# Performance work log

Measured on AMD Instinct MI355X. Metric: run time of the kernel, lower is better.

Reference implementation:

```python
import jax, jax.numpy as jnp
import numpy as np

N = 50000      # nodes
E = 500000     # edges (before self-loops)
D = 384        # in_channels == hidden3*6 (residual constraint)
H1, C1 = 4, 96   # conv1: heads, out_channels  -> 384
H2, C2 = 4, 96   # conv2 -> 384
H3, C3 = 6, 64   # conv3 -> 384
B = 64           # graphs in batch
SLOPE = 0.2      # GATConv leaky_relu negative_slope (PyG default)
LN_EPS = 1e-5


def _gat_params(key, fin, heads, c, scale=0.05):
    k1, k2, k3 = jax.random.split(key, 3)
    return dict(
        W=jax.random.normal(k1, (fin, heads * c), jnp.float32) * scale,
        a_src=jax.random.normal(k2, (heads, c), jnp.float32) * scale,
        a_dst=jax.random.normal(k3, (heads, c), jnp.float32) * scale,
        b=jnp.zeros((heads * c,), jnp.float32),
    )


def setup_inputs() -> dict:
    key = jax.random.key(0)
    ks = jax.random.split(key, 8)
    x = jax.random.normal(ks[0], (N, D), jnp.float32)
    edge_index = jax.random.randint(ks[1], (2, E), 0, N).astype(jnp.int64)
    batch = jnp.sort(jax.random.randint(ks[2], (N,), 0, B)).astype(jnp.int64)
    p1 = _gat_params(ks[3], D, H1, C1)
    p2 = _gat_params(ks[4], H1 * C1, H2, C2)
    p3 = _gat_params(ks[5], H2 * C2, H3, C3)
    return {
        'x': x, 'edge_index': edge_index, 'batch': batch,
        'W1': p1['W'], 'a1_src': p1['a_src'], 'a1_dst': p1['a_dst'], 'b1': p1['b'],
        'g1': jnp.ones((H1 * C1,), jnp.float32), 'be1': jnp.zeros((H1 * C1,), jnp.float32),
        'W2': p2['W'], 'a2_src': p2['a_src'], 'a2_dst': p2['a_dst'], 'b2': p2['b'],
        'g2': jnp.ones((H2 * C2,), jnp.float32), 'be2': jnp.zeros((H2 * C2,), jnp.float32),
        'W3': p3['W'], 'a3_src': p3['a_src'], 'a3_dst': p3['a_dst'], 'b3': p3['b'],
    }


def _layer_norm(x, g, b):
    mu = jnp.mean(x, axis=-1, keepdims=True)
    var = jnp.mean(jnp.square(x - mu), axis=-1, keepdims=True)
    return (x - mu) * jax.lax.rsqrt(var + LN_EPS) * g + b


def _gat_conv(x, src, dst, W, a_src, a_dst, b, heads, c):
    # h: [N, H, C] projected features (shared W across heads, PyG-style)
    h = (x @ W).reshape(N, heads, c)
    s_src = jnp.einsum('nhc,hc->nh', h, a_src)   # [N, H]
    s_dst = jnp.einsum('nhc,hc->nh', h, a_dst)
    e = jax.nn.leaky_relu(s_src[src] + s_dst[dst], SLOPE)  # [E', H]
    # segment softmax over incoming edges of each dst (self-loops guarantee coverage)
    e_max = jax.ops.segment_max(e, dst, num_segments=N)
    e = jnp.exp(e - e_max[dst])
    denom = jax.ops.segment_sum(e, dst, num_segments=N)
    alpha = e / (denom[dst] + 1e-16)                        # [E', H]
    out = jax.ops.segment_sum(h[src] * alpha[:, :, None], dst, num_segments=N)
    return out.reshape(N, heads * c) + b


def reference(x, edge_index, batch,
              W1, a1_src, a1_dst, b1, g1, be1,
              W2, a2_src, a2_dst, b2, g2, be2,
              W3, a3_src, a3_dst, b3):
    # PyG GATConv adds self-loops by default
    ar = jnp.arange(N, dtype=edge_index.dtype)
    ei = jnp.concatenate([edge_index, jnp.stack([ar, ar])], axis=1)
    src, dst = ei[0], ei[1]

    x1 = _gat_conv(x, src, dst, W1, a1_src, a1_dst, b1, H1, C1)
    x1 = jax.nn.relu(_layer_norm(x1, g1, be1))
    x2 = _gat_conv(x1, src, dst, W2, a2_src, a2_dst, b2, H2, C2)
    x2 = jax.nn.relu(_layer_norm(x2, g2, be2))
    x3 = _gat_conv(x2, src, dst, W3, a3_src, a3_dst, b3, H3, C3)
    x3 = jax.nn.relu(x3)

    x_res = x + x3
    # global_mean_pool over batch assignment (dropout is identity at eval)
    sums = jax.ops.segment_sum(x_res, batch, num_segments=B)
    counts = jax.ops.segment_sum(jnp.ones((N,), x.dtype), batch, num_segments=B)
    return sums / jnp.maximum(counts, 1.0)[:, None]
```

## Files before the change

### kernel.cpp

```cpp
#include <hip/hip_runtime.h>

#define NNODES 50000
#define NEDGES 500000
#define DIM    384
#define NB     64
#define SLOPE  0.2f
#define LN_EPS 1e-5f
#define EPRIME (NEDGES + NNODES)
#define POOLS  16
#define SCANB  256
#define NSCB   ((NNODES + SCANB - 1) / SCANB)

typedef __attribute__((ext_vector_type(8))) short short8;
typedef __attribute__((ext_vector_type(4))) float floatx4;
typedef __attribute__((ext_vector_type(2))) float floatx2;

__device__ __forceinline__ int load_i(const void* p, long long i, int is64) {
  return is64 ? (int)((const long long*)p)[i] : ((const int*)p)[i];
}
__device__ __forceinline__ unsigned short f2bf(float f) {
  unsigned u = __float_as_uint(f);
  u += 0x7fffu + ((u >> 16) & 1u);
  return (unsigned short)(u >> 16);
}
__device__ __forceinline__ float bf2f(unsigned short u) {
  return __uint_as_float(((unsigned)u) << 16);
}

__global__ void detect_kernel(const int* __restrict__ ei32, int* __restrict__ flag) {
  __shared__ int nz;
  if (threadIdx.x == 0) nz = 0;
  __syncthreads();
  if (ei32[2 * threadIdx.x + 1] != 0) atomicAdd(&nz, 1);
  __syncthreads();
  if (threadIdx.x == 0) *flag = (nz == 0) ? 1 : 0;
}

__global__ void count_kernel(const void* __restrict__ ei, const int* __restrict__ flag,
                             int* __restrict__ deg) {
  int is64 = *flag;
  for (int i = blockIdx.x * blockDim.x + threadIdx.x; i < EPRIME; i += gridDim.x * blockDim.x) {
    int d = (i < NEDGES) ? load_i(ei, (long long)NEDGES + i, is64) : (i - NEDGES);
    atomicAdd(&deg[d], 1);
  }
}

__global__ void scan1_kernel(const int* __restrict__ deg, int* __restrict__ row_ptr,
                             int* __restrict__ btot) {
  __shared__ int buf[SCANB];
  int t = threadIdx.x, idx = blockIdx.x * SCANB + t;
  int v = (idx < NNODES) ? deg[idx] : 0;
  buf[t] = v;
  __syncthreads();
  for (int off = 1; off < SCANB; off <<= 1) {
    int x = (t >= off) ? buf[t - off] : 0;
    __syncthreads();
    buf[t] += x;
    __syncthreads();
  }
  if (idx < NNODES) row_ptr[idx] = buf[t] - v;
  if (t == SCANB - 1) btot[blockIdx.x] = buf[t];
}
__global__ void scan2_kernel(int* __restrict__ btot) {
  __shared__ int buf[256];
  int t = threadIdx.x;
  int v = (t < NSCB) ? btot[t] : 0;
  buf[t] = v;
  __syncthreads();
  for (int off = 1; off < 256; off <<= 1) {
    int x = (t >= off) ? buf[t - off] : 0;
    __syncthreads();
    buf[t] += x;
    __syncthreads();
  }
  if (t < NSCB) btot[t] = buf[t] - v;
}
__global__ void scan3_kernel(int* __restrict__ row_ptr, int* __restrict__ cursor,
                             const int* __restrict__ btot) {
  int idx = blockIdx.x * SCANB + threadIdx.x;
  if (idx < NNODES) {
    int v = row_ptr[idx] + btot[blockIdx.x];
    row_ptr[idx] = v;
    cursor[idx] = v;
  }
  if (idx == 0) row_ptr[NNODES] = EPRIME;
}

__global__ void scatter_kernel(const void* __restrict__ ei, const int* __restrict__ flag,
                               int* __restrict__ cursor, int* __restrict__ srt) {
  int is64 = *flag;
  for (int i = blockIdx.x * blockDim.x + threadIdx.x; i < EPRIME; i += gridDim.x * blockDim.x) {
    int s, d;
    if (i < NEDGES) { s = load_i(ei, i, is64); d = load_i(ei, (long long)NEDGES + i, is64); }
    else            { s = d = i - NEDGES; }
    int pos = atomicAdd(&cursor[d], 1);
    srt[pos] = s;
  }
}

__global__ void convert_x_kernel(const float* __restrict__ x, unsigned short* __restrict__ xb) {
  int i = blockIdx.x * blockDim.x + threadIdx.x;
  float4 v = ((const float4*)x)[i];
  ushort4 o;
  o.x = f2bf(v.x); o.y = f2bf(v.y); o.z = f2bf(v.z); o.w = f2bf(v.w);
  ((ushort4*)xb)[i] = o;
}

__global__ void convert_w_kernel(const float* __restrict__ W1, const float* __restrict__ W2,
                                 const float* __restrict__ W3, unsigned short* __restrict__ Wt) {
  const float* W = (blockIdx.y == 0) ? W1 : (blockIdx.y == 1) ? W2 : W3;
  unsigned short* o = Wt + (size_t)blockIdx.y * DIM * DIM;
  int n = blockIdx.x;
  int k = threadIdx.x;
  o[n * DIM + k] = f2bf(W[k * DIM + n]);
}

__global__ __launch_bounds__(256)
void gemm_bf16_kernel(const unsigned short* __restrict__ A,
                      const unsigned short* __restrict__ Bt,
                      unsigned short* __restrict__ Cb, int M) {
  __shared__ unsigned short As[128 * 32];
  __shared__ unsigned short Bs[128 * 32];
  int tid = threadIdx.x;
  int lane = tid & 63;
  int wave = tid >> 6;
  int bm = blockIdx.x * 128;
  int bn = blockIdx.y * 128;
  int wm = (wave & 1) * 64;
  int wn = (wave >> 1) * 64;
  int l16 = lane & 15;
  int lq  = lane >> 4;

  floatx4 acc[4][4];
#pragma unroll
  for (int mi = 0; mi < 4; ++mi)
#pragma unroll
    for (int ni = 0; ni < 4; ++ni)
      acc[mi][ni] = (floatx4){0.f, 0.f, 0.f, 0.f};

  for (int k0 = 0; k0 < DIM; k0 += 32) {
    __syncthreads();
#pragma unroll
    for (int i = 0; i < 2; ++i) {
      int c = i * 256 + tid;
      int r = c >> 2;
      int col = (c & 3) << 3;
      int ra = bm + r; if (ra >= M) ra = M - 1;
      __builtin_amdgcn_global_load_lds(
          (const __attribute__((address_space(1))) void*)(A + (size_t)ra * DIM + k0 + col),
          (__attribute__((address_space(3))) void*)(As + c * 8), 16, 0, 0);
      __builtin_amdgcn_global_load_lds(
          (const __attribute__((address_space(1))) void*)(Bt + (size_t)(bn + r) * DIM + k0 + col),
          (__attribute__((address_space(3))) void*)(Bs + c * 8), 16, 0, 0);
    }
    __syncthreads();
    short8 av[4], bv[4];
#pragma unroll
    for (int mi = 0; mi < 4; ++mi)
      av[mi] = *(const short8*)&As[(wm + mi * 16 + l16) * 32 + lq * 8];
#pragma unroll
    for (int ni = 0; ni < 4; ++ni)
      bv[ni] = *(const short8*)&Bs[(wn + ni * 16 + l16) * 32 + lq * 8];
#pragma unroll
    for (int mi = 0; mi < 4; ++mi)
#pragma unroll
      for (int ni = 0; ni < 4; ++ni)
        acc[mi][ni] = __builtin_amdgcn_mfma_f32_16x16x32_bf16(av[mi], bv[ni], acc[mi][ni], 0, 0, 0);
  }

#pragma unroll
  for (int mi = 0; mi < 4; ++mi) {
#pragma unroll
    for (int r = 0; r < 4; ++r) {
      int row = bm + wm + mi * 16 + lq * 4 + r;
      if (row < M) {
#pragma unroll
        for (int ni = 0; ni < 4; ++ni)
          Cb[(size_t)row * DIM + bn + wn + ni * 16 + l16] = f2bf(acc[mi][ni][r]);
      }
    }
  }
}

template <int H>
__global__ __launch_bounds__(256)
void score_kernel(const unsigned short* __restrict__ hmat,
                  const float* __restrict__ asrc, const float* __restrict__ adst,
                  float* __restrict__ ssrc, float* __restrict__ sdst,
                  unsigned char* __restrict__ h8) {
  constexpr int LPH = 48 / H;
  int wave = threadIdx.x >> 6, lane = threadIdx.x & 63;
  int n = blockIdx.x * 4 + wave;
  bool colane = lane < 48;
  int lc = min(lane, 47);
  int j = lc * 8;

  __shared__ float r1[4][64], r2[4][64];
  float s1 = 0.f, s2 = 0.f;
  if (colane) {
    uint4 pk = *(const uint4*)(hmat + (size_t)n * DIM + j);
    float f[8];
    f[0] = __uint_as_float(pk.x << 16); f[1] = __uint_as_float(pk.x & 0xffff0000u);
    f[2] = __uint_as_float(pk.y << 16); f[3] = __uint_as_float(pk.y & 0xffff0000u);
    f[4] = __uint_as_float(pk.z << 16); f[5] = __uint_as_float(pk.z & 0xffff0000u);
    f[6] = __uint_as_float(pk.w << 16); f[7] = __uint_as_float(pk.w & 0xffff0000u);
    float4 a0 = *(const float4*)(asrc + j);
    float4 a1 = *(const float4*)(asrc + j + 4);
    float4 d0 = *(const float4*)(adst + j);
    float4 d1 = *(const float4*)(adst + j + 4);
    s1 = f[0]*a0.x + f[1]*a0.y + f[2]*a0.z + f[3]*a0.w
       + f[4]*a1.x + f[5]*a1.y + f[6]*a1.z + f[7]*a1.w;
    s2 = f[0]*d0.x + f[1]*d0.y + f[2]*d0.z + f[3]*d0.w
       + f[4]*d1.x + f[5]*d1.y + f[6]*d1.z + f[7]*d1.w;
    int w0 = __builtin_amdgcn_cvt_pk_fp8_f32(f[0], f[1], 0, false);
    w0 = __builtin_amdgcn_cvt_pk_fp8_f32(f[2], f[3], w0, true);
    int w1 = __builtin_amdgcn_cvt_pk_fp8_f32(f[4], f[5], 0, false);
    w1 = __builtin_amdgcn_cvt_pk_fp8_f32(f[6], f[7], w1, true);
    uint2 st; st.x = (unsigned)w0; st.y = (unsigned)w1;
    *(uint2*)(h8 + (size_t)n * DIM + j) = st;
  }
  r1[wave][lane] = colane ? s1 : 0.f;
  r2[wave][lane] = colane ? s2 : 0.f;
  asm volatile("s_waitcnt lgkmcnt(0)" ::: "memory");
  __builtin_amdgcn_wave_barrier();
  if (lane < H) {
    float a = 0.f;
#pragma unroll
    for (int k = 0; k < LPH; ++k) a += r1[wave][lane * LPH + k];
    ssrc[n * H + lane] = a;
  } else if (lane >= 8 && lane < 8 + H) {
    int h = lane - 8;
    float a = 0.f;
#pragma unroll
    for (int k = 0; k < LPH; ++k) a += r2[wave][h * LPH + k];
    sdst[n * H + h] = a;
  }
}

template <int H>
__global__ __launch_bounds__(256)
void softmax_kernel(const int* __restrict__ row_ptr, const int* __restrict__ srt,
                    const float* __restrict__ ssrc, const float* __restrict__ sdst,
                    float* __restrict__ alpha) {
  int idx = blockIdx.x * 256 + threadIdx.x;
  if (idx >= NNODES * H) return;
  int n = idx / H, h = idx - n * H;
  int start = row_ptr[n], end = row_ptr[n + 1];
  float sd = sdst[n * H + h];
  float den = 0.f;
  for (int e = start; e < end; ++e) {
    float v = ssrc[srt[e] * H + h] + sd;
    v = fmaxf(v, SLOPE * v);
    den += __expf(v);
  }
  float inv = 1.f / (den + 1e-16f);
  for (int e = start; e < end; ++e) {
    float v = ssrc[srt[e] * H + h] + sd;
    v = fmaxf(v, SLOPE * v);
    alpha[(size_t)e * H + h] = __expf(v) * inv;
  }
}

template <int H, int MODE>
__global__ __launch_bounds__(256)
void aggregate_kernel(const int* __restrict__ row_ptr, const int* __restrict__ srt,
                      const float* __restrict__ alpha,
                      const unsigned char* __restrict__ h8, const float* __restrict__ bias,
                      const float* __restrict__ gamma, const float* __restrict__ beta,
                      const unsigned short* __restrict__ xresb,
                      unsigned short* __restrict__ outb) {
  constexpr int C = DIM / H;
  int wave = threadIdx.x >> 6;
  int lane = threadIdx.x & 63;
  int n = blockIdx.x * 4 + wave;
  int start = row_ptr[n];
  int deg = row_ptr[n + 1] - start;

  bool colane = lane < 48;
  int lc = min(lane, 47);
  int j = lc * 8;
  int myhead = j / C;

  float acc[8];
#pragma unroll
  for (int i = 0; i < 8; ++i) acc[i] = 0.f;

  const int* sp = srt + start;
  const float* ap = alpha + (size_t)start * H + myhead;

  auto accum = [&](uint2 pk, float w) {
    floatx2 p0 = __builtin_amdgcn_cvt_pk_f32_fp8((int)pk.x, false);
    floatx2 p1 = __builtin_amdgcn_cvt_pk_f32_fp8((int)pk.x, true);
    floatx2 p2 = __builtin_amdgcn_cvt_pk_f32_fp8((int)pk.y, false);
    floatx2 p3 = __builtin_amdgcn_cvt_pk_f32_fp8((int)pk.y, true);
    acc[0] = fmaf(w, p0.x, acc[0]); acc[1] = fmaf(w, p0.y, acc[1]);
    acc[2] = fmaf(w, p1.x, acc[2]); acc[3] = fmaf(w, p1.y, acc[3]);
    acc[4] = fmaf(w, p2.x, acc[4]); acc[5] = fmaf(w, p2.y, acc[5]);
    acc[6] = fmaf(w, p3.x, acc[6]); acc[7] = fmaf(w, p3.y, acc[7]);
  };

  int ee = 0;
  for (; ee + 4 <= deg; ee += 4) {
    int i0 = sp[ee], i1 = sp[ee + 1], i2 = sp[ee + 2], i3 = sp[ee + 3];
    int s0 = __builtin_amdgcn_readfirstlane(i0);
    int s1 = __builtin_amdgcn_readfirstlane(i1);
    int s2 = __builtin_amdgcn_readfirstlane(i2);
    int s3 = __builtin_amdgcn_readfirstlane(i3);
    uint2 k0 = *(const uint2*)(h8 + (size_t)s0 * DIM + j);
    uint2 k1 = *(const uint2*)(h8 + (size_t)s1 * DIM + j);
    uint2 k2 = *(const uint2*)(h8 + (size_t)s2 * DIM + j);
    uint2 k3 = *(const uint2*)(h8 + (size_t)s3 * DIM + j);
    float w0 = ap[(ee) * H];
    float w1 = ap[(ee + 1) * H];
    float w2 = ap[(ee + 2) * H];
    float w3 = ap[(ee + 3) * H];
    accum(k0, w0); accum(k1, w1); accum(k2, w2); accum(k3, w3);
  }
  for (; ee < deg; ++ee) {
    int su = __builtin_amdgcn_readfirstlane(sp[ee]);
    uint2 pk = *(const uint2*)(h8 + (size_t)su * DIM + j);
    accum(pk, ap[ee * H]);
  }

  float v[8];
  float4 b0 = *(const float4*)(bias + j);
  float4 b1 = *(const float4*)(bias + j + 4);
  v[0] = acc[0] + b0.x; v[1] = acc[1] + b0.y;
  v[2] = acc[2] + b0.z; v[3] = acc[3] + b0.w;
  v[4] = acc[4] + b1.x; v[5] = acc[5] + b1.y;
  v[6] = acc[6] + b1.z; v[7] = acc[7] + b1.w;

  if (MODE == 0) {
    float s1 = 0.f, s2 = 0.f;
    if (colane) {
#pragma unroll
      for (int i = 0; i < 8; ++i) { s1 += v[i]; s2 += v[i] * v[i]; }
    }
#pragma unroll
    for (int off = 32; off > 0; off >>= 1) {
      s1 += __shfl_xor(s1, off);
      s2 += __shfl_xor(s2, off);
    }
    float mu = s1 * (1.f / DIM);
    float var = s2 * (1.f / DIM) - mu * mu;
    float rs = rsqrtf(var + LN_EPS);
    if (colane) {
      float4 g0 = *(const float4*)(gamma + j);
      float4 g1 = *(const float4*)(gamma + j + 4);
      float4 e0 = *(const float4*)(beta + j);
      float4 e1 = *(const float4*)(beta + j + 4);
      float gg[8] = {g0.x, g0.y, g0.z, g0.w, g1.x, g1.y, g1.z, g1.w};
      float bb[8] = {e0.x, e0.y, e0.z, e0.w, e1.x, e1.y, e1.z, e1.w};
      ushort4 o0, o1;
      unsigned short oy[8];
#pragma unroll
      for (int i = 0; i < 8; ++i) {
        float y = (v[i] - mu) * rs * gg[i] + bb[i];
        oy[i] = f2bf(fmaxf(y, 0.f));
      }
      o0.x = oy[0]; o0.y = oy[1]; o0.z = oy[2]; o0.w = oy[3];
      o1.x = oy[4]; o1.y = oy[5]; o1.z = oy[6]; o1.w = oy[7];
      *(ushort4*)(outb + (size_t)n * DIM + j) = o0;
      *(ushort4*)(outb + (size_t)n * DIM + j + 4) = o1;
    }
  } else {
    if (colane) {
      uint4 xp = *(const uint4*)(xresb + (size_t)n * DIM + j);
      float xf[8];
      xf[0] = __uint_as_float(xp.x << 16); xf[1] = __uint_as_float(xp.x & 0xffff0000u);
      xf[2] = __uint_as_float(xp.y << 16); xf[3] = __uint_as_float(xp.y & 0xffff0000u);
      xf[4] = __uint_as_float(xp.z << 16); xf[5] = __uint_as_float(xp.z & 0xffff0000u);
      xf[6] = __uint_as_float(xp.w << 16); xf[7] = __uint_as_float(xp.w & 0xffff0000u);
      ushort4 o0, o1;
      unsigned short oy[8];
#pragma unroll
      for (int i = 0; i < 8; ++i) oy[i] = f2bf(fmaxf(v[i], 0.f) + xf[i]);
      o0.x = oy[0]; o0.y = oy[1]; o0.z = oy[2]; o0.w = oy[3];
      o1.x = oy[4]; o1.y = oy[5]; o1.z = oy[6]; o1.w = oy[7];
      *(ushort4*)(outb + (size_t)n * DIM + j) = o0;
      *(ushort4*)(outb + (size_t)n * DIM + j + 4) = o1;
    }
  }
}

__global__ void pool_kernel(const unsigned short* __restrict__ xr, const void* __restrict__ batch,
                            const int* __restrict__ flag, float* __restrict__ out) {
  int b = blockIdx.x;
  int s = blockIdx.y;
  int t = threadIdx.x;
  int is64 = *flag;
  int lo, hi;
  { int l = 0, r = NNODES;
    while (l < r) { int m = (l + r) >> 1; if (load_i(batch, m, is64) < b) l = m + 1; else r = m; }
    lo = l; }
  { int l = lo, r = NNODES;
    while (l < r) { int m = (l + r) >> 1; if (load_i(batch, m, is64) < b + 1) l = m + 1; else r = m; }
    hi = l; }
  int cnt = hi - lo;
  float inv = 1.f / (float)max(cnt, 1);
  int chunk = (cnt + POOLS - 1) / POOLS;
  int r0 = lo + s * chunk;
  int r1 = min(r0 + chunk, hi);
  float acc = 0.f;
  for (int nn = r0; nn < r1; ++nn) acc += bf2f(xr[(size_t)nn * DIM + t]);
  if (r1 > r0) atomicAdd(&out[b * DIM + t], acc * inv);
}

extern "C" void kernel_launch(void* const* d_in, const int* in_sizes, int n_in,
                              void* d_out, int out_size, void* d_ws, size_t ws_size,
                              hipStream_t stream) {
  const float* x    = (const float*)d_in[0];
  const void*  ei   = d_in[1];
  const void*  batch= d_in[2];
  const float* W1   = (const float*)d_in[3];
  const float* a1s  = (const float*)d_in[4];
  const float* a1d  = (const float*)d_in[5];
  const float* b1   = (const float*)d_in[6];
  const float* g1   = (const float*)d_in[7];
  const float* be1  = (const float*)d_in[8];
  const float* W2   = (const float*)d_in[9];
  const float* a2s  = (const float*)d_in[10];
  const float* a2d  = (const float*)d_in[11];
  const float* b2   = (const float*)d_in[12];
  const float* g2   = (const float*)d_in[13];
  const float* be2  = (const float*)d_in[14];
  const float* W3   = (const float*)d_in[15];
  const float* a3s  = (const float*)d_in[16];
  const float* a3d  = (const float*)d_in[17];
  const float* b3   = (const float*)d_in[18];
  float* out = (float*)d_out;

  char* ws = (char*)d_ws;
  size_t off = 0;
  auto alloc = [&](size_t bytes) -> void* {
    void* p = ws + off;
    off = (off + bytes + 255) & ~(size_t)255;
    return p;
  };
  int*   flag    = (int*)alloc(4);
  unsigned short* Xb = (unsigned short*)alloc((size_t)NNODES * DIM * 2);
  unsigned short* Qb = (unsigned short*)alloc((size_t)NNODES * DIM * 2);
  unsigned short* P = (unsigned short*)alloc((size_t)NNODES * DIM * 2);
  unsigned char*  P8 = (unsigned char*)alloc((size_t)NNODES * DIM);
  unsigned short* Wt = (unsigned short*)alloc((size_t)3 * DIM * DIM * 2);
  float* ssrc    = (float*)alloc((size_t)NNODES * 6 * 4);
  float* sdst    = (float*)alloc((size_t)NNODES * 6 * 4);
  float* alpha   = (float*)alloc((size_t)EPRIME * 6 * 4);
  int*   row_ptr = (int*)alloc((size_t)(NNODES + 1) * 4);
  int*   cursor  = (int*)alloc((size_t)NNODES * 4);
  int*   deg     = (int*)alloc((size_t)NNODES * 4);
  int*   btot    = (int*)alloc((size_t)NSCB * 4);
  int*   srt     = (int*)alloc((size_t)EPRIME * 4);

  detect_kernel<<<1, 256, 0, stream>>>((const int*)ei, flag);
  hipMemsetAsync(deg, 0, (size_t)NNODES * 4, stream);
  hipMemsetAsync(d_out, 0, (size_t)out_size * 4, stream);
  int eblocks = (EPRIME + 255) / 256;
  count_kernel<<<eblocks, 256, 0, stream>>>(ei, flag, deg);
  scan1_kernel<<<NSCB, SCANB, 0, stream>>>(deg, row_ptr, btot);
  scan2_kernel<<<1, 256, 0, stream>>>(btot);
  scan3_kernel<<<NSCB, SCANB, 0, stream>>>(row_ptr, cursor, btot);
  scatter_kernel<<<eblocks, 256, 0, stream>>>(ei, flag, cursor, srt);

  convert_x_kernel<<<(NNODES * DIM / 4 + 255) / 256, 256, 0, stream>>>(x, Xb);
  convert_w_kernel<<<dim3(DIM, 3), DIM, 0, stream>>>(W1, W2, W3, Wt);

  dim3 ggrid((NNODES + 127) / 128, DIM / 128);
  int agrid = NNODES / 4;
  int smb4 = (NNODES * 4 + 255) / 256;
  int smb6 = (NNODES * 6 + 255) / 256;

  gemm_bf16_kernel<<<ggrid, 256, 0, stream>>>(Xb, Wt, P, NNODES);
  score_kernel<4><<<agrid, 256, 0, stream>>>(P, a1s, a1d, ssrc, sdst, P8);
  softmax_kernel<4><<<smb4, 256, 0, stream>>>(row_ptr, srt, ssrc, sdst, alpha);
  aggregate_kernel<4, 0><<<agrid, 256, 0, stream>>>(row_ptr, srt, alpha, P8, b1, g1, be1,
                                                    nullptr, Qb);
  gemm_bf16_kernel<<<ggrid, 256, 0, stream>>>(Qb, Wt + (size_t)DIM * DIM, P, NNODES);
  score_kernel<4><<<agrid, 256, 0, stream>>>(P, a2s, a2d, ssrc, sdst, P8);
  softmax_kernel<4><<<smb4, 256, 0, stream>>>(row_ptr, srt, ssrc, sdst, alpha);
  aggregate_kernel<4, 0><<<agrid, 256, 0, stream>>>(row_ptr, srt, alpha, P8, b2, g2, be2,
                                                    nullptr, Qb);
  gemm_bf16_kernel<<<ggrid, 256, 0, stream>>>(Qb, Wt + (size_t)2 * DIM * DIM, P, NNODES);
  score_kernel<6><<<agrid, 256, 0, stream>>>(P, a3s, a3d, ssrc, sdst, P8);
  softmax_kernel<6><<<smb6, 256, 0, stream>>>(row_ptr, srt, ssrc, sdst, alpha);
  aggregate_kernel<6, 1><<<agrid, 256, 0, stream>>>(row_ptr, srt, alpha, P8, b3, nullptr,
                                                    nullptr, Xb, Qb);
  pool_kernel<<<dim3(NB, POOLS), DIM, 0, stream>>>(Qb, batch, flag, out);
}
```

Baseline: 559.8 us.

## Write GEMM output as fp8 directly and defer softmax normalization to aggregate

The GEMM epilogue now writes fp8 bytes directly instead of a bf16 intermediate. The score kernel reads that fp8 buffer and no longer re-encodes it, which removes a full bf16 write and read per layer. The softmax kernel becomes a single pass that stores the unnormalized exponentials and a per-node denominator. The aggregate kernel divides by that denominator at the end, removing the second gather pass over edges. Costs: attention scores are now computed from fp8-rounded features, the GEMM writes single bytes per lane (narrow, poorly coalesced stores), and unnormalized exponentials could lose range without max subtraction.

```diff
diff --git a/kernel.cpp b/kernel.cpp
--- a/kernel.cpp
+++ b/kernel.cpp
@@ -118,7 +118,7 @@
 __global__ __launch_bounds__(256)
 void gemm_bf16_kernel(const unsigned short* __restrict__ A,
                       const unsigned short* __restrict__ Bt,
-                      unsigned short* __restrict__ Cb, int M) {
+                      unsigned char* __restrict__ C8, int M) {
   __shared__ unsigned short As[128 * 32];
   __shared__ unsigned short Bs[128 * 32];
   int tid = threadIdx.x;
@@ -175,8 +175,11 @@
       int row = bm + wm + mi * 16 + lq * 4 + r;
       if (row < M) {
 #pragma unroll
-        for (int ni = 0; ni < 4; ++ni)
-          Cb[(size_t)row * DIM + bn + wn + ni * 16 + l16] = f2bf(acc[mi][ni][r]);
+        for (int ni = 0; ni < 4; ++ni) {
+          float fv = acc[mi][ni][r];
+          int pk = __builtin_amdgcn_cvt_pk_fp8_f32(fv, fv, 0, false);
+          C8[(size_t)row * DIM + bn + wn + ni * 16 + l16] = (unsigned char)(pk & 0xff);
+        }
       }
     }
   }
@@ -184,10 +187,9 @@
 
 template <int H>
 __global__ __launch_bounds__(256)
-void score_kernel(const unsigned short* __restrict__ hmat,
+void score_kernel(const unsigned char* __restrict__ h8,
                   const float* __restrict__ asrc, const float* __restrict__ adst,
-                  float* __restrict__ ssrc, float* __restrict__ sdst,
-                  unsigned char* __restrict__ h8) {
+                  float* __restrict__ ssrc, float* __restrict__ sdst) {
   constexpr int LPH = 48 / H;
   int wave = threadIdx.x >> 6, lane = threadIdx.x & 63;
   int n = blockIdx.x * 4 + wave;
@@ -198,12 +200,12 @@
   __shared__ float r1[4][64], r2[4][64];
   float s1 = 0.f, s2 = 0.f;
   if (colane) {
-    uint4 pk = *(const uint4*)(hmat + (size_t)n * DIM + j);
-    float f[8];
-    f[0] = __uint_as_float(pk.x << 16); f[1] = __uint_as_float(pk.x & 0xffff0000u);
-    f[2] = __uint_as_float(pk.y << 16); f[3] = __uint_as_float(pk.y & 0xffff0000u);
-    f[4] = __uint_as_float(pk.z << 16); f[5] = __uint_as_float(pk.z & 0xffff0000u);
-    f[6] = __uint_as_float(pk.w << 16); f[7] = __uint_as_float(pk.w & 0xffff0000u);
+    uint2 pk = *(const uint2*)(h8 + (size_t)n * DIM + j);
+    floatx2 p0 = __builtin_amdgcn_cvt_pk_f32_fp8((int)pk.x, false);
+    floatx2 p1 = __builtin_amdgcn_cvt_pk_f32_fp8((int)pk.x, true);
+    floatx2 p2 = __builtin_amdgcn_cvt_pk_f32_fp8((int)pk.y, false);
+    floatx2 p3 = __builtin_amdgcn_cvt_pk_f32_fp8((int)pk.y, true);
+    float f[8] = {p0.x, p0.y, p1.x, p1.y, p2.x, p2.y, p3.x, p3.y};
     float4 a0 = *(const float4*)(asrc + j);
     float4 a1 = *(const float4*)(asrc + j + 4);
     float4 d0 = *(const float4*)(adst + j);
@@ -212,12 +214,6 @@
        + f[4]*a1.x + f[5]*a1.y + f[6]*a1.z + f[7]*a1.w;
     s2 = f[0]*d0.x + f[1]*d0.y + f[2]*d0.z + f[3]*d0.w
        + f[4]*d1.x + f[5]*d1.y + f[6]*d1.z + f[7]*d1.w;
-    int w0 = __builtin_amdgcn_cvt_pk_fp8_f32(f[0], f[1], 0, false);
-    w0 = __builtin_amdgcn_cvt_pk_fp8_f32(f[2], f[3], w0, true);
-    int w1 = __builtin_amdgcn_cvt_pk_fp8_f32(f[4], f[5], 0, false);
-    w1 = __builtin_amdgcn_cvt_pk_fp8_f32(f[6], f[7], w1, true);
-    uint2 st; st.x = (unsigned)w0; st.y = (unsigned)w1;
-    *(uint2*)(h8 + (size_t)n * DIM + j) = st;
   }
   r1[wave][lane] = colane ? s1 : 0.f;
   r2[wave][lane] = colane ? s2 : 0.f;
@@ -239,9 +235,9 @@
 
 template <int H>
 __global__ __launch_bounds__(256)
-void softmax_kernel(const int* __restrict__ row_ptr, const int* __restrict__ srt,
-                    const float* __restrict__ ssrc, const float* __restrict__ sdst,
-                    float* __restrict__ alpha) {
+void wexp_kernel(const int* __restrict__ row_ptr, const int* __restrict__ srt,
+                 const float* __restrict__ ssrc, const float* __restrict__ sdst,
+                 float* __restrict__ walpha, float* __restrict__ dden) {
   int idx = blockIdx.x * 256 + threadIdx.x;
   if (idx >= NNODES * H) return;
   int n = idx / H, h = idx - n * H;
@@ -251,20 +247,17 @@
   for (int e = start; e < end; ++e) {
     float v = ssrc[srt[e] * H + h] + sd;
     v = fmaxf(v, SLOPE * v);
-    den += __expf(v);
-  }
-  float inv = 1.f / (den + 1e-16f);
-  for (int e = start; e < end; ++e) {
-    float v = ssrc[srt[e] * H + h] + sd;
-    v = fmaxf(v, SLOPE * v);
-    alpha[(size_t)e * H + h] = __expf(v) * inv;
-  }
+    float w = __expf(v);
+    walpha[(size_t)e * H + h] = w;
+    den += w;
+  }
+  dden[n * H + h] = den;
 }
 
 template <int H, int MODE>
 __global__ __launch_bounds__(256)
 void aggregate_kernel(const int* __restrict__ row_ptr, const int* __restrict__ srt,
-                      const float* __restrict__ alpha,
+                      const float* __restrict__ walpha, const float* __restrict__ dden,
                       const unsigned char* __restrict__ h8, const float* __restrict__ bias,
                       const float* __restrict__ gamma, const float* __restrict__ beta,
                       const unsigned short* __restrict__ xresb,
@@ -281,12 +274,14 @@
   int j = lc * 8;
   int myhead = j / C;
 
+  float invden = 1.f / (dden[n * H + myhead] + 1e-16f);
+
   float acc[8];
 #pragma unroll
   for (int i = 0; i < 8; ++i) acc[i] = 0.f;
 
   const int* sp = srt + start;
-  const float* ap = alpha + (size_t)start * H + myhead;
+  const float* ap = walpha + (size_t)start * H + myhead;
 
   auto accum = [&](uint2 pk, float w) {
     floatx2 p0 = __builtin_amdgcn_cvt_pk_f32_fp8((int)pk.x, false);
@@ -325,10 +320,10 @@
   float v[8];
   float4 b0 = *(const float4*)(bias + j);
   float4 b1 = *(const float4*)(bias + j + 4);
-  v[0] = acc[0] + b0.x; v[1] = acc[1] + b0.y;
-  v[2] = acc[2] + b0.z; v[3] = acc[3] + b0.w;
-  v[4] = acc[4] + b1.x; v[5] = acc[5] + b1.y;
-  v[6] = acc[6] + b1.z; v[7] = acc[7] + b1.w;
+  v[0] = acc[0] * invden + b0.x; v[1] = acc[1] * invden + b0.y;
+  v[2] = acc[2] * invden + b0.z; v[3] = acc[3] * invden + b0.w;
+  v[4] = acc[4] * invden + b1.x; v[5] = acc[5] * invden + b1.y;
+  v[6] = acc[6] * invden + b1.z; v[7] = acc[7] * invden + b1.w;
 
   if (MODE == 0) {
     float s1 = 0.f, s2 = 0.f;
@@ -440,12 +435,12 @@
   int*   flag    = (int*)alloc(4);
   unsigned short* Xb = (unsigned short*)alloc((size_t)NNODES * DIM * 2);
   unsigned short* Qb = (unsigned short*)alloc((size_t)NNODES * DIM * 2);
-  unsigned short* P = (unsigned short*)alloc((size_t)NNODES * DIM * 2);
   unsigned char*  P8 = (unsigned char*)alloc((size_t)NNODES * DIM);
   unsigned short* Wt = (unsigned short*)alloc((size_t)3 * DIM * DIM * 2);
   float* ssrc    = (float*)alloc((size_t)NNODES * 6 * 4);
   float* sdst    = (float*)alloc((size_t)NNODES * 6 * 4);
-  float* alpha   = (float*)alloc((size_t)EPRIME * 6 * 4);
+  float* walpha  = (float*)alloc((size_t)EPRIME * 6 * 4);
+  float* dden    = (float*)alloc((size_t)NNODES * 6 * 4);
   int*   row_ptr = (int*)alloc((size_t)(NNODES + 1) * 4);
   int*   cursor  = (int*)alloc((size_t)NNODES * 4);
   int*   deg     = (int*)alloc((size_t)NNODES * 4);
@@ -470,20 +465,20 @@
   int smb4 = (NNODES * 4 + 255) / 256;
   int smb6 = (NNODES * 6 + 255) / 256;
 
-  gemm_bf16_kernel<<<ggrid, 256, 0, stream>>>(Xb, Wt, P, NNODES);
-  score_kernel<4><<<agrid, 256, 0, stream>>>(P, a1s, a1d, ssrc, sdst, P8);
-  softmax_kernel<4><<<smb4, 256, 0, stream>>>(row_ptr, srt, ssrc, sdst, alpha);
-  aggregate_kernel<4, 0><<<agrid, 256, 0, stream>>>(row_ptr, srt, alpha, P8, b1, g1, be1,
+  gemm_bf16_kernel<<<ggrid, 256, 0, stream>>>(Xb, Wt, P8, NNODES);
+  score_kernel<4><<<agrid, 256, 0, stream>>>(P8, a1s, a1d, ssrc, sdst);
+  wexp_kernel<4><<<smb4, 256, 0, stream>>>(row_ptr, srt, ssrc, sdst, walpha, dden);
+  aggregate_kernel<4, 0><<<agrid, 256, 0, stream>>>(row_ptr, srt, walpha, dden, P8, b1, g1, be1,
                                                     nullptr, Qb);
-  gemm_bf16_kernel<<<ggrid, 256, 0, stream>>>(Qb, Wt + (size_t)DIM * DIM, P, NNODES);
-  score_kernel<4><<<agrid, 256, 0, stream>>>(P, a2s, a2d, ssrc, sdst, P8);
-  softmax_kernel<4><<<smb4, 256, 0, stream>>>(row_ptr, srt, ssrc, sdst, alpha);
-  aggregate_kernel<4, 0><<<agrid, 256, 0, stream>>>(row_ptr, srt, alpha, P8, b2, g2, be2,
+  gemm_bf16_kernel<<<ggrid, 256, 0, stream>>>(Qb, Wt + (size_t)DIM * DIM, P8, NNODES);
+  score_kernel<4><<<agrid, 256, 0, stream>>>(P8, a2s, a2d, ssrc, sdst);
+  wexp_kernel<4><<<smb4, 256, 0, stream>>>(row_ptr, srt, ssrc, sdst, walpha, dden);
+  aggregate_kernel<4, 0><<<agrid, 256, 0, stream>>>(row_ptr, srt, walpha, dden, P8, b2, g2, be2,
                                                     nullptr, Qb);
-  gemm_bf16_kernel<<<ggrid, 256, 0, stream>>>(Qb, Wt + (size_t)2 * DIM * DIM, P, NNODES);
-  score_kernel<6><<<agrid, 256, 0, stream>>>(P, a3s, a3d, ssrc, sdst, P8);
-  softmax_kernel<6><<<smb6, 256, 0, stream>>>(row_ptr, srt, ssrc, sdst, alpha);
-  aggregate_kernel<6, 1><<<agrid, 256, 0, stream>>>(row_ptr, srt, alpha, P8, b3, nullptr,
+  gemm_bf16_kernel<<<ggrid, 256, 0, stream>>>(Qb, Wt + (size_t)2 * DIM * DIM, P8, NNODES);
+  score_kernel<6><<<agrid, 256, 0, stream>>>(P8, a3s, a3d, ssrc, sdst);
+  wexp_kernel<6><<<smb6, 256, 0, stream>>>(row_ptr, srt, ssrc, sdst, walpha, dden);
+  aggregate_kernel<6, 1><<<agrid, 256, 0, stream>>>(row_ptr, srt, walpha, dden, P8, b3, nullptr,
                                                     nullptr, Xb, Qb);
   pool_kernel<<<dim3(NB, POOLS), DIM, 0, stream>>>(Qb, batch, flag, out);
 }
```

New measurement: 525.0 us. 6.2% less time.
